# Kernel optimization log

Measured on AMD Instinct MI355X. Metric: run time of the kernel, lower is better.

Reference implementation:

```python
import jax, jax.numpy as jnp
import numpy as np


def setup_inputs() -> dict:
    key = jax.random.key(0)
    k1, k2 = jax.random.split(key)
    H, W, C = 1024, 2048, 32
    img = jax.random.normal(k1, (1, C, H, W), dtype=jnp.float32)
    flow = jax.random.normal(k2, (1, 2, H, W), dtype=jnp.float32)
    return {"img": img, "flow": flow, "H": H, "W": W}


def reference(img, flow, H, W):
    # img: [1, C, H, W], flow: [1, 2, H, W]
    C = img.shape[1]
    u = flow[:, 0, :, :]  # [1, H, W]
    v = flow[:, 1, :, :]
    grid_x = jnp.arange(W, dtype=jnp.float32)[None, None, :]  # [1,1,W]
    grid_y = jnp.arange(H, dtype=jnp.float32)[None, :, None]  # [1,H,1]
    x = grid_x + u  # [1, H, W]
    y = grid_y + v
    # normalize to [-1, 1] then back (faithful to original two-step mapping)
    x = 2.0 * (x / (W - 1) - 0.5)
    y = 2.0 * (y / (H - 1) - 0.5)
    x = (x + 1.0) * 0.5 * (W - 1)
    y = (y + 1.0) * 0.5 * (H - 1)

    x0 = jnp.floor(x)
    x1 = x0 + 1.0
    y0 = jnp.floor(y)
    y1 = y0 + 1.0
    x0c = jnp.clip(x0, 0, W - 1).astype(jnp.int32)
    x1c = jnp.clip(x1, 0, W - 1).astype(jnp.int32)
    y0c = jnp.clip(y0, 0, H - 1).astype(jnp.int32)
    y1c = jnp.clip(y1, 0, H - 1).astype(jnp.int32)

    # bilinear weights from UNCLAMPED coords (as in the original)
    wa = (x1 - x) * (y1 - y)
    wb = (x1 - x) * (y - y0)
    wc = (x - x0) * (y1 - y)
    wd = (x - x0) * (y - y0)

    img_flat = jnp.transpose(img[0], (1, 2, 0)).reshape(H * W, C)  # [H*W, C]

    def gather_pixel(ix, iy):
        idx = (iy * W + ix).reshape(-1)  # [H*W]
        return jnp.take(img_flat, idx, axis=0)  # [H*W, C]

    Ia = gather_pixel(x0c, y0c)
    Ib = gather_pixel(x0c, y1c)
    Ic = gather_pixel(x1c, y0c)
    Id = gather_pixel(x1c, y1c)

    out = (Ia * wa.reshape(-1, 1) + Ib * wb.reshape(-1, 1)
           + Ic * wc.reshape(-1, 1) + Id * wd.reshape(-1, 1))  # [H*W, C]
    out = out.reshape(1, H, W, C)
    return jnp.transpose(out, (0, 3, 1, 2))  # [1, C, H, W]
```

## Files before the change

### kernel.cpp

```cpp
#include <hip/hip_runtime.h>


#define TSX 64
#define TSY 32
#define RAD 8
#define LW  80
#define LH  48
#define PLANE (LW*LH)
#define CG  4
#define KROWS 2
#define NTHREADS 1024

#define GLOAD_LDS16(g, l)                                                  \
    __builtin_amdgcn_global_load_lds(                                      \
        (const __attribute__((address_space(1))) void*)(g),                \
        (__attribute__((address_space(3))) void*)(l), 16, 0, 0)

__global__ __launch_bounds__(NTHREADS, 8) void warp_lds_dma2(
    const float* __restrict__ img,
    const float* __restrict__ flow,
    const int* __restrict__ Hp,
    const int* __restrict__ Wp,
    float* __restrict__ out,
    int HW, int C, int NCG)
{
    __shared__ __align__(16) float lds[CG * PLANE];

    const int W = *Wp;
    const int H = *Hp;
    const int tilesX = (W + TSX - 1) / TSX;
    const int tilesY = (H + TSY - 1) / TSY;
    const int ntiles = tilesX * tilesY;

    const int cg = blockIdx.x % NCG;
    const int t  = blockIdx.x / NCG;
    if (t >= ntiles) return;

    const int tileY = t / tilesX;
    const int tileX = t - tileY * tilesX;
    const int gx0 = tileX * TSX - RAD;
    const int gy0 = tileY * TSY - RAD;

    const int tid = threadIdx.x;
    const int lx  = tid & 63;
    const int rw  = (tid >> 6) * KROWS;

    const int c0 = cg * CG;
    const int nc = min(CG, C - c0);

    const float Wm1 = (float)(W - 1);
    const float Hm1 = (float)(H - 1);
    const int gx = tileX * TSX + lx;

    float w0[KROWS], w1[KROWS], w2[KROWS], w3[KROWS];
    int   enc[KROWS];
    int   pixk[KROWS];
    #pragma unroll
    for (int k = 0; k < KROWS; ++k) {
        const int gy = tileY * TSY + rw + k;
        if (gx >= W || gy >= H) { enc[k] = -2; continue; }
        const int pix = gy * W + gx;
        pixk[k] = pix;
        const float u = flow[pix];
        const float v = flow[HW + pix];

        const float x = (float)gx + u;
        const float y = (float)gy + v;

        const float x0 = floorf(x), x1 = x0 + 1.0f;
        const float y0 = floorf(y), y1 = y0 + 1.0f;

        const int x0c = (int)fminf(fmaxf(x0, 0.0f), Wm1);
        const int x1c = (int)fminf(fmaxf(x1, 0.0f), Wm1);
        const int y0c = (int)fminf(fmaxf(y0, 0.0f), Hm1);
        const int y1c = (int)fminf(fmaxf(y1, 0.0f), Hm1);

        const float wa = (x1 - x) * (y1 - y);
        const float wb = (x1 - x) * (y - y0);
        const float wc = (x - x0) * (y1 - y);
        const float wd = (x - x0) * (y - y0);

        const int pb = min(x0c, W - 2);
        w0[k] = (x0c == pb ? wa : 0.0f) + (x1c == pb ? wc : 0.0f);
        w1[k] = (x0c != pb ? wa : 0.0f) + (x1c != pb ? wc : 0.0f);
        w2[k] = (x0c == pb ? wb : 0.0f) + (x1c == pb ? wd : 0.0f);
        w3[k] = (x0c != pb ? wb : 0.0f) + (x1c != pb ? wd : 0.0f);

        const int lxp = pb - gx0;
        const int ly0 = y0c - gy0;
        const int ly1 = y1c - gy0;
        if (lxp >= 0 && lxp + 1 < LW && ly0 >= 0 && ly1 < LH) {
            enc[k] = (ly0 * LW + lxp) | ((ly1 - ly0) << 12);
        } else {
            enc[k] = -1;
        }
    }

    const bool xint = (gx0 >= 0) && (gx0 + LW <= W) && ((W & 3) == 0);
    if (xint) {
        const int NV = LH * (LW / 4);
        for (int i = tid; i < nc * NV; i += NTHREADS) {
            const int ch  = i / NV;
            const int rem = i - ch * NV;
            const int r   = rem / (LW / 4);
            const int g   = rem - r * (LW / 4);
            const int yy  = min(max(gy0 + r, 0), H - 1);
            const float* src = img + (size_t)(c0 + ch) * HW
                                   + (size_t)yy * W + (gx0 + 4 * g);
            GLOAD_LDS16(src, &lds[i * 4]);
        }
    } else {
        for (int i = tid; i < nc * PLANE; i += NTHREADS) {
            const int ch  = i / PLANE;
            const int rem = i - ch * PLANE;
            const int r   = rem / LW;
            const int cc  = rem - r * LW;
            const int yy  = min(max(gy0 + r, 0), H - 1);
            const int xx  = min(max(gx0 + cc, 0), W - 1);
            lds[i] = img[(size_t)(c0 + ch) * HW + (size_t)yy * W + xx];
        }
    }

    __syncthreads();

    #pragma unroll
    for (int k = 0; k < KROWS; ++k) {
        const int e = enc[k];
        if (e == -2) continue;

        if (__builtin_expect(e >= 0, 1)) {
            const float* bt = lds + (e & 4095);
            const float* bb = bt + ((e >> 12) & 1) * LW;
            float* o = out + (size_t)c0 * (size_t)HW + pixk[k];
            const float a0 = w0[k], a1 = w1[k], a2 = w2[k], a3 = w3[k];
            if (nc == CG) {
                #pragma unroll
                for (int c = 0; c < CG; ++c) {
                    const float lt = bt[c * PLANE], ht = bt[c * PLANE + 1];
                    const float lb = bb[c * PLANE], hb = bb[c * PLANE + 1];
                    o[(size_t)c * (size_t)HW] = a0*lt + a1*ht + a2*lb + a3*hb;
                }
            } else {
                for (int c = 0; c < nc; ++c) {
                    const float lt = bt[c * PLANE], ht = bt[c * PLANE + 1];
                    const float lb = bb[c * PLANE], hb = bb[c * PLANE + 1];
                    o[(size_t)c * (size_t)HW] = a0*lt + a1*ht + a2*lb + a3*hb;
                }
            }
        } else {
            const int pix = pixk[k];
            const int gy  = tileY * TSY + rw + k;
            const float u = flow[pix];
            const float v = flow[HW + pix];
            const float x = (float)gx + u;
            const float y = (float)gy + v;
            const float x0 = floorf(x), y0f = floorf(y);
            const int x0c = (int)fminf(fmaxf(x0, 0.0f), Wm1);
            const int x1c = (int)fminf(fmaxf(x0 + 1.0f, 0.0f), Wm1);
            const int y0c = (int)fminf(fmaxf(y0f, 0.0f), Hm1);
            const int y1c = (int)fminf(fmaxf(y0f + 1.0f, 0.0f), Hm1);
            const float wa = (x0 + 1.0f - x) * (y0f + 1.0f - y);
            const float wb = (x0 + 1.0f - x) * (y - y0f);
            const float wc = (x - x0) * (y0f + 1.0f - y);
            const float wd = (x - x0) * (y - y0f);
            for (int c = 0; c < nc; ++c) {
                const float* ic = img + (size_t)(c0 + c) * HW;
                const float Ia = ic[(size_t)y0c * W + x0c];
                const float Ib = ic[(size_t)y1c * W + x0c];
                const float Ic = ic[(size_t)y0c * W + x1c];
                const float Id = ic[(size_t)y1c * W + x1c];
                out[(size_t)(c0 + c) * HW + pix] = wa*Ia + wb*Ib + wc*Ic + wd*Id;
            }
        }
    }
}

extern "C" void kernel_launch(void* const* d_in, const int* in_sizes, int n_in,
                              void* d_out, int out_size, void* d_ws, size_t ws_size,
                              hipStream_t stream) {
    const float* img  = (const float*)d_in[0];
    const float* flow = (const float*)d_in[1];
    const int*   Hp   = (const int*)d_in[2];
    const int*   Wp   = (const int*)d_in[3];
    float* out = (float*)d_out;

    const int HW = in_sizes[1] / 2;
    const int C  = in_sizes[0] / HW;
    const int NCG = (C + CG - 1) / CG;

    const int maxt = (HW + TSX * TSY - 1) / (TSX * TSY) + 1024;
    const int grid = maxt * NCG;
    warp_lds_dma2<<<grid, NTHREADS, 0, stream>>>(img, flow, Hp, Wp, out, HW, C, NCG);
}
```

Baseline: 150.7 us.

## Loop over channel pairs per tile with double-buffered LDS DMA prefetch

Each block now handles one spatial tile across all channels, two channels per phase. The next phase's halo is prefetched into a second LDS buffer by async global-to-LDS loads while the current phase is computed. Flow and weight setup run once per tile instead of once per channel group, and tiles are remapped so each XCD gets a contiguous range. The cost is far fewer blocks (one per tile) and a barrier every phase, which may limit parallelism and latency hiding.

```diff
diff --git a/kernel.cpp b/kernel.cpp
--- a/kernel.cpp
+++ b/kernel.cpp
@@ -7,8 +7,8 @@
 #define LW  80
 #define LH  48
 #define PLANE (LW*LH)
-#define CG  4
-#define KROWS 2
+#define CGB 2
+#define NV (LH*(LW/4))
 #define NTHREADS 1024
 
 #define GLOAD_LDS16(g, l)                                                  \
@@ -16,25 +16,27 @@
         (const __attribute__((address_space(1))) void*)(g),                \
         (__attribute__((address_space(3))) void*)(l), 16, 0, 0)
 
-__global__ __launch_bounds__(NTHREADS, 8) void warp_lds_dma2(
+__global__ __launch_bounds__(NTHREADS, 8) void warp_pipe(
     const float* __restrict__ img,
     const float* __restrict__ flow,
     const int* __restrict__ Hp,
     const int* __restrict__ Wp,
     float* __restrict__ out,
-    int HW, int C, int NCG)
+    int HW, int C)
 {
-    __shared__ __align__(16) float lds[CG * PLANE];
+    __shared__ __align__(16) float lds[2][CGB * PLANE];
 
     const int W = *Wp;
     const int H = *Hp;
     const int tilesX = (W + TSX - 1) / TSX;
     const int tilesY = (H + TSY - 1) / TSY;
     const int ntiles = tilesX * tilesY;
+    const int bid = blockIdx.x;
+    if (bid >= ntiles) return;
 
-    const int cg = blockIdx.x % NCG;
-    const int t  = blockIdx.x / NCG;
-    if (t >= ntiles) return;
+    const int q = ntiles >> 3, r = ntiles & 7;
+    const int xcd = bid & 7, sub = bid >> 3;
+    const int t = (xcd < r ? xcd * (q + 1) : r * (q + 1) + (xcd - r) * q) + sub;
 
     const int tileY = t / tilesX;
     const int tileX = t - tileY * tilesX;
@@ -43,22 +45,19 @@
 
     const int tid = threadIdx.x;
     const int lx  = tid & 63;
-    const int rw  = (tid >> 6) * KROWS;
-
-    const int c0 = cg * CG;
-    const int nc = min(CG, C - c0);
+    const int rw  = (tid >> 6) * 2;
+    const int gx  = tileX * TSX + lx;
 
     const float Wm1 = (float)(W - 1);
     const float Hm1 = (float)(H - 1);
-    const int gx = tileX * TSX + lx;
 
-    float w0[KROWS], w1[KROWS], w2[KROWS], w3[KROWS];
-    int   enc[KROWS];
-    int   pixk[KROWS];
+    float wtl[2], wth[2], wbl[2], wbh[2];
+    int   enc[2], pixk[2];
     #pragma unroll
-    for (int k = 0; k < KROWS; ++k) {
+    for (int k = 0; k < 2; ++k) {
         const int gy = tileY * TSY + rw + k;
-        if (gx >= W || gy >= H) { enc[k] = -2; continue; }
+        enc[k] = -2;
+        if (gx >= W || gy >= H) continue;
         const int pix = gy * W + gx;
         pixk[k] = pix;
         const float u = flow[pix];
@@ -66,7 +65,6 @@
 
         const float x = (float)gx + u;
         const float y = (float)gy + v;
-
         const float x0 = floorf(x), x1 = x0 + 1.0f;
         const float y0 = floorf(y), y1 = y0 + 1.0f;
 
@@ -80,98 +78,104 @@
         const float wc = (x - x0) * (y1 - y);
         const float wd = (x - x0) * (y - y0);
 
-        const int pb = min(x0c, W - 2);
-        w0[k] = (x0c == pb ? wa : 0.0f) + (x1c == pb ? wc : 0.0f);
-        w1[k] = (x0c != pb ? wa : 0.0f) + (x1c != pb ? wc : 0.0f);
-        w2[k] = (x0c == pb ? wb : 0.0f) + (x1c == pb ? wd : 0.0f);
-        w3[k] = (x0c != pb ? wb : 0.0f) + (x1c != pb ? wd : 0.0f);
+        const int pbx = min(x0c, W - 2);
+        const int pby = min(y0c, H - 2);
 
-        const int lxp = pb - gx0;
-        const int ly0 = y0c - gy0;
-        const int ly1 = y1c - gy0;
-        if (lxp >= 0 && lxp + 1 < LW && ly0 >= 0 && ly1 < LH) {
-            enc[k] = (ly0 * LW + lxp) | ((ly1 - ly0) << 12);
-        } else {
-            enc[k] = -1;
-        }
+        const float wlt = (x0c == pbx ? wa : 0.f) + (x1c == pbx ? wc : 0.f);
+        const float wht = (x0c != pbx ? wa : 0.f) + (x1c != pbx ? wc : 0.f);
+        const float wlb = (x0c == pbx ? wb : 0.f) + (x1c == pbx ? wd : 0.f);
+        const float whb = (x0c != pbx ? wb : 0.f) + (x1c != pbx ? wd : 0.f);
+        const bool t0 = (y0c == pby), t1 = (y1c == pby);
+        wtl[k] = (t0 ? wlt : 0.f) + (t1 ? wlb : 0.f);
+        wth[k] = (t0 ? wht : 0.f) + (t1 ? whb : 0.f);
+        wbl[k] = (t0 ? 0.f : wlt) + (t1 ? 0.f : wlb);
+        wbh[k] = (t0 ? 0.f : wht) + (t1 ? 0.f : whb);
+
+        const int lxp = pbx - gx0;
+        const int lyb = pby - gy0;
+        enc[k] = (lxp >= 0 && lxp <= LW - 2 && lyb >= 0 && lyb <= LH - 2)
+               ? (lyb * LW + lxp) : -1;
     }
 
-    const bool xint = (gx0 >= 0) && (gx0 + LW <= W) && ((W & 3) == 0);
-    if (xint) {
-        const int NV = LH * (LW / 4);
-        for (int i = tid; i < nc * NV; i += NTHREADS) {
-            const int ch  = i / NV;
-            const int rem = i - ch * NV;
-            const int r   = rem / (LW / 4);
-            const int g   = rem - r * (LW / 4);
-            const int yy  = min(max(gy0 + r, 0), H - 1);
-            const float* src = img + (size_t)(c0 + ch) * HW
-                                   + (size_t)yy * W + (gx0 + 4 * g);
-            GLOAD_LDS16(src, &lds[i * 4]);
-        }
-    } else {
-        for (int i = tid; i < nc * PLANE; i += NTHREADS) {
-            const int ch  = i / PLANE;
-            const int rem = i - ch * PLANE;
-            const int r   = rem / LW;
-            const int cc  = rem - r * LW;
-            const int yy  = min(max(gy0 + r, 0), H - 1);
-            const int xx  = min(max(gx0 + cc, 0), W - 1);
-            lds[i] = img[(size_t)(c0 + ch) * HW + (size_t)yy * W + xx];
-        }
+    const int nph = (C + CGB - 1) / CGB;
+
+    for (int i = tid; i < CGB * NV; i += NTHREADS) {
+        const int ch  = i / NV;
+        const int rem = i - ch * NV;
+        const int rr  = rem / (LW / 4);
+        const int g   = rem - rr * (LW / 4);
+        const int yy  = min(max(gy0 + rr, 0), H - 1);
+        const int xs  = min(max(gx0 + 4 * g, 0), W - 4);
+        const int chc = min(ch, C - 1);
+        GLOAD_LDS16(img + (size_t)chc * HW + (size_t)yy * W + xs,
+                    &lds[0][i * 4]);
     }
 
-    __syncthreads();
+    int buf = 0;
+    for (int p = 0; p < nph; ++p) {
+        __syncthreads();
 
-    #pragma unroll
-    for (int k = 0; k < KROWS; ++k) {
-        const int e = enc[k];
-        if (e == -2) continue;
+        const int c0 = p * CGB;
 
-        if (__builtin_expect(e >= 0, 1)) {
-            const float* bt = lds + (e & 4095);
-            const float* bb = bt + ((e >> 12) & 1) * LW;
-            float* o = out + (size_t)c0 * (size_t)HW + pixk[k];
-            const float a0 = w0[k], a1 = w1[k], a2 = w2[k], a3 = w3[k];
-            if (nc == CG) {
+        if (p + 1 < nph) {
+            const int c0n = (p + 1) * CGB;
+            float* dst = &lds[buf ^ 1][0];
+            for (int i = tid; i < CGB * NV; i += NTHREADS) {
+                const int ch  = i / NV;
+                const int rem = i - ch * NV;
+                const int rr  = rem / (LW / 4);
+                const int g   = rem - rr * (LW / 4);
+                const int yy  = min(max(gy0 + rr, 0), H - 1);
+                const int xs  = min(max(gx0 + 4 * g, 0), W - 4);
+                const int chc = min(c0n + ch, C - 1);
+                GLOAD_LDS16(img + (size_t)chc * HW + (size_t)yy * W + xs,
+                            dst + i * 4);
+            }
+        }
+
+        const float* base = &lds[buf][0];
+        #pragma unroll
+        for (int k = 0; k < 2; ++k) {
+            const int e = enc[k];
+            if (e == -2) continue;
+
+            if (__builtin_expect(e >= 0, 1)) {
+                const float* b0 = base + e;
                 #pragma unroll
-                for (int c = 0; c < CG; ++c) {
-                    const float lt = bt[c * PLANE], ht = bt[c * PLANE + 1];
-                    const float lb = bb[c * PLANE], hb = bb[c * PLANE + 1];
-                    o[(size_t)c * (size_t)HW] = a0*lt + a1*ht + a2*lb + a3*hb;
+                for (int c = 0; c < CGB; ++c) {
+                    if (c0 + c >= C) break;
+                    const float lt = b0[c * PLANE],      ht = b0[c * PLANE + 1];
+                    const float lb = b0[c * PLANE + LW], hb = b0[c * PLANE + LW + 1];
+                    out[(size_t)(c0 + c) * HW + pixk[k]] =
+                        wtl[k] * lt + wth[k] * ht + wbl[k] * lb + wbh[k] * hb;
                 }
             } else {
-                for (int c = 0; c < nc; ++c) {
-                    const float lt = bt[c * PLANE], ht = bt[c * PLANE + 1];
-                    const float lb = bb[c * PLANE], hb = bb[c * PLANE + 1];
-                    o[(size_t)c * (size_t)HW] = a0*lt + a1*ht + a2*lb + a3*hb;
+                const int pix = pixk[k];
+                const int gy  = tileY * TSY + rw + k;
+                const float u = flow[pix];
+                const float v = flow[HW + pix];
+                const float x = (float)gx + u;
+                const float y = (float)gy + v;
+                const float x0 = floorf(x), y0f = floorf(y);
+                const int x0c = (int)fminf(fmaxf(x0, 0.0f), Wm1);
+                const int x1c = (int)fminf(fmaxf(x0 + 1.0f, 0.0f), Wm1);
+                const int y0c = (int)fminf(fmaxf(y0f, 0.0f), Hm1);
+                const int y1c = (int)fminf(fmaxf(y0f + 1.0f, 0.0f), Hm1);
+                const float wa = (x0 + 1.0f - x) * (y0f + 1.0f - y);
+                const float wb = (x0 + 1.0f - x) * (y - y0f);
+                const float wc = (x - x0) * (y0f + 1.0f - y);
+                const float wd = (x - x0) * (y - y0f);
+                for (int c = 0; c < CGB && c0 + c < C; ++c) {
+                    const float* ic = img + (size_t)(c0 + c) * HW;
+                    const float Ia = ic[(size_t)y0c * W + x0c];
+                    const float Ib = ic[(size_t)y1c * W + x0c];
+                    const float Ic = ic[(size_t)y0c * W + x1c];
+                    const float Id = ic[(size_t)y1c * W + x1c];
+                    out[(size_t)(c0 + c) * HW + pix] = wa*Ia + wb*Ib + wc*Ic + wd*Id;
                 }
             }
-        } else {
-            const int pix = pixk[k];
-            const int gy  = tileY * TSY + rw + k;
-            const float u = flow[pix];
-            const float v = flow[HW + pix];
-            const float x = (float)gx + u;
-            const float y = (float)gy + v;
-            const float x0 = floorf(x), y0f = floorf(y);
-            const int x0c = (int)fminf(fmaxf(x0, 0.0f), Wm1);
-            const int x1c = (int)fminf(fmaxf(x0 + 1.0f, 0.0f), Wm1);
-            const int y0c = (int)fminf(fmaxf(y0f, 0.0f), Hm1);
-            const int y1c = (int)fminf(fmaxf(y0f + 1.0f, 0.0f), Hm1);
-            const float wa = (x0 + 1.0f - x) * (y0f + 1.0f - y);
-            const float wb = (x0 + 1.0f - x) * (y - y0f);
-            const float wc = (x - x0) * (y0f + 1.0f - y);
-            const float wd = (x - x0) * (y - y0f);
-            for (int c = 0; c < nc; ++c) {
-                const float* ic = img + (size_t)(c0 + c) * HW;
-                const float Ia = ic[(size_t)y0c * W + x0c];
-                const float Ib = ic[(size_t)y1c * W + x0c];
-                const float Ic = ic[(size_t)y0c * W + x1c];
-                const float Id = ic[(size_t)y1c * W + x1c];
-                out[(size_t)(c0 + c) * HW + pix] = wa*Ia + wb*Ib + wc*Ic + wd*Id;
-            }
         }
+        buf ^= 1;
     }
 }
 
@@ -186,9 +190,7 @@
 
     const int HW = in_sizes[1] / 2;
     const int C  = in_sizes[0] / HW;
-    const int NCG = (C + CG - 1) / CG;
 
-    const int maxt = (HW + TSX * TSY - 1) / (TSX * TSY) + 1024;
-    const int grid = maxt * NCG;
-    warp_lds_dma2<<<grid, NTHREADS, 0, stream>>>(img, flow, Hp, Wp, out, HW, C, NCG);
+    const int grid = (HW + TSX * TSY - 1) / (TSX * TSY) + 64;
+    warp_pipe<<<grid, NTHREADS, 0, stream>>>(img, flow, Hp, Wp, out, HW, C);
 }
```

Measured after the change: 132.3 us. -12.2%, faster.
